# Kernel tuning notes

Hardware: AMD Instinct MI355X
Metric: run time of the kernel (lower is better)

Reference implementation:

```python
import jax, jax.numpy as jnp
import numpy as np

C = 512
NUM_HEADS = 4
GROUPS = 32
EPS = 1e-5


def setup_inputs() -> dict:
    key = jax.random.key(0)
    ks = jax.random.split(key, 7)
    x = jax.random.normal(ks[0], (1, C, 4, 32, 32), dtype=jnp.float32)
    norm_w = jax.random.normal(ks[1], (C,), dtype=jnp.float32) * 0.02 + 1.0
    norm_b = jax.random.normal(ks[2], (C,), dtype=jnp.float32) * 0.02
    # 1x1x1 Conv3d == pointwise linear over channels
    qkv_w = jax.random.normal(ks[3], (3 * C, C), dtype=jnp.float32) * (C ** -0.5)
    qkv_b = jax.random.normal(ks[4], (3 * C,), dtype=jnp.float32) * 0.02
    proj_w = jax.random.normal(ks[5], (C, C), dtype=jnp.float32) * (C ** -0.5)
    proj_b = jax.random.normal(ks[6], (C,), dtype=jnp.float32) * 0.02
    return {"x": x, "norm_w": norm_w, "norm_b": norm_b,
            "qkv_w": qkv_w, "qkv_b": qkv_b,
            "proj_w": proj_w, "proj_b": proj_b}


def reference(x, norm_w, norm_b, qkv_w, qkv_b, proj_w, proj_b):
    B, Cc, T, H, W = x.shape
    N = T * H * W
    nh = NUM_HEADS
    d = Cc // nh
    # GroupNorm(32, C), biased variance, eps=1e-5
    xg = x.reshape(B, GROUPS, Cc // GROUPS, N)
    mu = xg.mean(axis=(2, 3), keepdims=True)
    var = xg.var(axis=(2, 3), keepdims=True)
    h = ((xg - mu) * jax.lax.rsqrt(var + EPS)).reshape(B, Cc, N)
    h = h * norm_w[None, :, None] + norm_b[None, :, None]
    # QKV 1x1 conv as channel matmul: (B, 3C, N)
    qkv = jnp.einsum('oc,bcn->bon', qkv_w, h) + qkv_b[None, :, None]
    qkv = qkv.reshape(B, 3, nh, d, N)
    q, k, v = qkv[:, 0], qkv[:, 1], qkv[:, 2]  # each (B, nh, d, N)
    scale = d ** -0.5
    attn = jax.nn.softmax(jnp.einsum('bhdn,bhdm->bhnm', q, k) * scale, axis=-1)
    out = jnp.einsum('bhnm,bhdm->bhdn', attn, v).reshape(B, Cc, N)
    out = jnp.einsum('oc,bcn->bon', proj_w, out) + proj_b[None, :, None]
    return x + out.reshape(B, Cc, T, H, W)
```

## Files before the change

### kernel.cpp

```cpp
#include <hip/hip_runtime.h>
#include <hip/hip_bf16.h>

#define CDIM 512
#define NTOK 4096
#define NH 4
#define DH 128
#define NGRP 32
#define EPS 1e-5f
#define NSPLIT 4
#define KVBLK 64
#define TPS (NTOK/KVBLK/NSPLIT)

typedef __attribute__((ext_vector_type(8))) short bf16x8;
typedef __attribute__((ext_vector_type(4))) short short4v;
typedef __attribute__((ext_vector_type(4))) float f32x4;
typedef __attribute__((ext_vector_type(16))) float f32x16;
typedef __attribute__((ext_vector_type(2))) unsigned int u32x2;

__device__ inline unsigned short f2bf(float f){
  unsigned int u = __float_as_uint(f);
  u = (u + 0x7fffu + ((u >> 16) & 1u)) >> 16;
  return (unsigned short)u;
}

__device__ inline float bf2f(unsigned short u){
  return __uint_as_float(((unsigned int)u) << 16);
}

__device__ inline f32x4 mfma_bf16(bf16x8 a, bf16x8 b, f32x4 c){
  asm("v_mfma_f32_16x16x32_bf16 %0, %1, %2, %0" : "+v"(c) : "v"(a), "v"(b));
  return c;
}

__device__ inline f32x16 mfma32(bf16x8 a, bf16x8 b, f32x16 c){
  asm("v_mfma_f32_32x32x16_bf16 %0, %1, %2, %0" : "+v"(c) : "v"(a), "v"(b));
  return c;
}

__device__ inline unsigned int cvtpk(float lo, float hi){
  unsigned int r;
  asm("v_cvt_pk_bf16_f32 %0, %1, %2" : "=v"(r) : "v"(lo), "v"(hi));
  return r;
}

#define GLD16(gsrc, ldst) \
  __builtin_amdgcn_global_load_lds((__attribute__((address_space(1))) const void*)(gsrc), \
                                   (__attribute__((address_space(3))) void*)(ldst), 16, 0, 0)

#define KSC (0.088388347648318447f * 1.4426950408889634f)
#define INV_KSC (1.0f / KSC)
#define THR_RAW 60.0f
#define THR_K (THR_RAW * KSC)

__global__ __launch_bounds__(256) void k_convert(const float* __restrict__ qkv_w,
                                                 const float* __restrict__ proj_w,
                                                 unsigned short* __restrict__ qw,
                                                 unsigned short* __restrict__ pw){
  int stride = gridDim.x * blockDim.x;
  int i0 = blockIdx.x * blockDim.x + threadIdx.x;
  for (int i = i0; i < 3*CDIM*CDIM; i += stride) qw[i] = f2bf(qkv_w[i]);
  for (int i = i0; i < CDIM*CDIM; i += stride)   pw[i] = f2bf(proj_w[i]);
}

__global__ __launch_bounds__(256) void k_gnstats(const float* __restrict__ x,
                                                 float* __restrict__ stats){
  const int g = blockIdx.x, t = threadIdx.x;
  const f32x4* p = (const f32x4*)(x + (size_t)g * (16*NTOK));
  float s = 0.f, ss = 0.f;
  for (int i = t; i < 16*NTOK/4; i += 256){
    f32x4 v = p[i];
    s  += v[0]+v[1]+v[2]+v[3];
    ss += v[0]*v[0]+v[1]*v[1]+v[2]*v[2]+v[3]*v[3];
  }
  for (int off = 32; off > 0; off >>= 1){ s += __shfl_down(s, off); ss += __shfl_down(ss, off); }
  __shared__ float rs[4], rss[4];
  if ((t & 63) == 0){ rs[t>>6] = s; rss[t>>6] = ss; }
  __syncthreads();
  if (t == 0){
    float S  = rs[0]+rs[1]+rs[2]+rs[3];
    float SS = rss[0]+rss[1]+rss[2]+rss[3];
    const float inv = 1.f / (float)(16*NTOK);
    float mu  = S * inv;
    float var = SS * inv - mu*mu;
    stats[g]        = mu;
    stats[NGRP + g] = rsqrtf(var + EPS);
  }
}

__global__ __launch_bounds__(256) void k_gnapply(const float* __restrict__ x,
                                                 const float* __restrict__ stats,
                                                 const float* __restrict__ nw,
                                                 const float* __restrict__ nbias,
                                                 unsigned short* __restrict__ h_t){
  __shared__ float tile[64][68];
  const int n0 = blockIdx.x * 64, c0 = blockIdx.y * 64;
  const int t = threadIdx.x;
  {
    const int cl = t >> 2;
    #pragma unroll
    for (int i = 0; i < 4; i++){
      const int f4 = (t & 3) + i*4;
      *(f32x4*)&tile[cl][f4*4] = *(const f32x4*)(x + (size_t)(c0+cl)*NTOK + n0 + f4*4);
    }
  }
  __syncthreads();
  const int nl = t >> 2, cb = (t & 3) * 16;
  unsigned short ov[16] __attribute__((aligned(8)));
  #pragma unroll
  for (int j = 0; j < 16; j++){
    const int c = c0 + cb + j;
    const int grp = c >> 4;
    const float val = (tile[cb+j][nl] - stats[grp]) * stats[NGRP+grp] * nw[c] + nbias[c];
    ov[j] = f2bf(val);
  }
  unsigned short* dst = h_t + (size_t)(n0+nl)*CDIM + c0 + cb;
  #pragma unroll
  for (int j = 0; j < 4; j++) *(short4v*)(dst + j*4) = *(const short4v*)(ov + j*4);
}

template<int MODE>
__global__ __launch_bounds__(256) void k_gemm(const unsigned short* __restrict__ A,
                                              const unsigned short* __restrict__ Bt,
                                              const float* __restrict__ bias,
                                              const float* __restrict__ xres,
                                              unsigned short* __restrict__ q_t,
                                              unsigned short* __restrict__ k_t,
                                              unsigned short* __restrict__ vbuf,
                                              float* __restrict__ out,
                                              int K)
{
  __shared__ unsigned short Asm[128*32];
  __shared__ unsigned short Bsm[128*32];
  const int m0 = blockIdx.y * 128, n0 = blockIdx.x * 128;
  const int t = threadIdx.x;
  const int lane = t & 63, w = t >> 6;
  const int lo = lane & 15, g = lane >> 4;
  const int wr = w >> 1, wc = w & 1;
  f32x4 acc[4][4];
  #pragma unroll
  for (int i=0;i<4;i++)
    #pragma unroll
    for (int j=0;j<4;j++) acc[i][j] = f32x4{0.f,0.f,0.f,0.f};

  const int row = t >> 2, cb8 = (t & 3) * 8;
  for (int k0 = 0; k0 < K; k0 += 32){
    __syncthreads();
    *(bf16x8*)(Asm + row*32 + cb8)      = *(const bf16x8*)(A  + (size_t)(m0+row)*K    + k0 + cb8);
    *(bf16x8*)(Asm + (row+64)*32 + cb8) = *(const bf16x8*)(A  + (size_t)(m0+row+64)*K + k0 + cb8);
    *(bf16x8*)(Bsm + row*32 + cb8)      = *(const bf16x8*)(Bt + (size_t)(n0+row)*K    + k0 + cb8);
    *(bf16x8*)(Bsm + (row+64)*32 + cb8) = *(const bf16x8*)(Bt + (size_t)(n0+row+64)*K + k0 + cb8);
    __syncthreads();
    bf16x8 af[4], bfr[4];
    #pragma unroll
    for (int i=0;i<4;i++) af[i]  = *(const bf16x8*)(Asm + (wr*64 + i*16 + lo)*32 + g*8);
    #pragma unroll
    for (int j=0;j<4;j++) bfr[j] = *(const bf16x8*)(Bsm + (wc*64 + j*16 + lo)*32 + g*8);
    #pragma unroll
    for (int i=0;i<4;i++)
      #pragma unroll
      for (int j=0;j<4;j++)
        acc[i][j] = mfma_bf16(af[i], bfr[j], acc[i][j]);
  }

  if constexpr (MODE == 0){
    const int sQ = m0 >> 9;
    const int hh = (m0 >> 7) & 3;
    #pragma unroll
    for (int i=0;i<4;i++){
      const int ddb = wr*64 + i*16 + g*4;
      const int ob  = m0 + ddb;
      float b[4];
      #pragma unroll
      for (int r=0;r<4;r++) b[r] = bias[ob + r];
      #pragma unroll
      for (int j=0;j<4;j++){
        const int n = n0 + wc*64 + j*16 + lo;
        if (sQ < 2){
          unsigned short pk[4] __attribute__((aligned(8)));
          #pragma unroll
          for (int r=0;r<4;r++) pk[r] = f2bf(acc[i][j][r] + b[r]);
          unsigned short* dst = (sQ == 0 ? q_t : k_t) + ((size_t)hh*NTOK + n)*DH + ddb;
          *(short4v*)dst = *(const short4v*)pk;
        } else {
          #pragma unroll
          for (int r=0;r<4;r++)
            vbuf[((size_t)hh*DH + ddb + r)*NTOK + n] = f2bf(acc[i][j][r] + b[r]);
        }
      }
    }
  } else {
    #pragma unroll
    for (int i=0;i<4;i++){
      const int ob = m0 + wr*64 + i*16 + g*4;
      float b[4];
      #pragma unroll
      for (int r=0;r<4;r++) b[r] = bias[ob + r];
      #pragma unroll
      for (int j=0;j<4;j++){
        const int n = n0 + wc*64 + j*16 + lo;
        #pragma unroll
        for (int r=0;r<4;r++){
          size_t idx = (size_t)(ob + r)*NTOK + n;
          out[idx] = acc[i][j][r] + b[r] + xres[idx];
        }
      }
    }
  }
}

__global__ __launch_bounds__(256, 2) void k_attn(const unsigned short* __restrict__ q_t,
                                                 const unsigned short* __restrict__ k_t,
                                                 const unsigned short* __restrict__ vbuf,
                                                 unsigned short* __restrict__ opart,
                                                 float* __restrict__ mlbuf){
  const int h = blockIdx.y;
  const int qt = blockIdx.x >> 2, split = blockIdx.x & 3;
  const int t = threadIdx.x, w = t >> 6, lane = t & 63;
  const int la = lane & 31, hi = lane >> 5;
  const int s15 = la & 15, s7 = la & 7;
  const int nbq = qt * 128 + w * 32;

  __shared__ __align__(16) unsigned short Ksm[64*128];
  __shared__ __align__(16) unsigned short Vsm[128*64];
  __shared__ __align__(16) unsigned short Pt[4][32][76];

  const unsigned short* kg = k_t  + (size_t)h*NTOK*DH;
  const unsigned short* vg = vbuf + (size_t)h*DH*NTOK;

  auto stage = [&](int mt){
    const unsigned short* kgm = kg + (size_t)mt*KVBLK*DH;
    const unsigned short* vgm = vg + mt*KVBLK;
    #pragma unroll
    for (int rnd = 0; rnd < 4; rnd++){
      const int c = rnd*256 + t;
      const int row = c >> 4, col = c & 15;
      GLD16(kgm + (size_t)row*DH + ((col ^ (row & 15))*8), &Ksm[c*8]);
    }
    #pragma unroll
    for (int rnd = 0; rnd < 4; rnd++){
      const int c = rnd*256 + t;
      const int row = c >> 3, col = c & 7;
      GLD16(vgm + (size_t)row*NTOK + ((col ^ (row & 7))*8), &Vsm[c*8]);
    }
  };

  bf16x8 qa[8];
  {
    const unsigned short* qr = q_t + ((size_t)h*NTOK + nbq + la)*DH + hi*8;
    #pragma unroll
    for (int ks=0;ks<8;ks++) qa[ks] = *(const bf16x8*)(qr + ks*16);
  }

  float mk = -1e30f;
  float lsum = 0.f;
  f32x16 oacc[4];
  #pragma unroll
  for (int dt=0;dt<4;dt++)
    #pragma unroll
    for (int r=0;r<16;r++) oacc[dt][r] = 0.f;

  const int mt0 = split * TPS;
  for (int it = 0; it < TPS; it++){
    __syncthreads();
    stage(mt0 + it);
    __syncthreads();

    const unsigned short* Ks = Ksm;
    const unsigned short* Vs = Vsm;
    unsigned short* Pw = &Pt[w][0][0];

    #pragma unroll
    for (int half = 0; half < 2; half++){
      f32x16 s;
      #pragma unroll
      for (int r=0;r<16;r++) s[r] = 0.f;
      __builtin_amdgcn_s_setprio(1);
      #pragma unroll
      for (int ks=0; ks<8; ks++){
        bf16x8 kf = *(const bf16x8*)(Ks + (half*32 + la)*128 + (((2*ks + hi) ^ s15) * 8));
        s = mfma32(kf, qa[ks], s);
      }
      __builtin_amdgcn_s_setprio(0);
      float hmax = s[0];
      #pragma unroll
      for (int r=1;r<16;r++) hmax = fmaxf(hmax, s[r]);
      hmax = fmaxf(hmax, __shfl_xor(hmax, 32));
      const float hk = hmax * KSC;
      if (!__all(hk <= mk + THR_K)){
        const float mnk = fmaxf(mk, hk);
        const float al  = exp2f(mk - mnk);
        mk = mnk;
        lsum *= al;
        #pragma unroll
        for (int dt=0;dt<4;dt++)
          #pragma unroll
          for (int r=0;r<16;r++) oacc[dt][r] *= al;
      }
      #pragma unroll
      for (int r=0;r<16;r++){
        s[r] = exp2f(fmaf(s[r], KSC, -mk));
        lsum += s[r];
      }
      #pragma unroll
      for (int g2=0; g2<4; g2++){
        u32x2 pk;
        pk[0] = cvtpk(s[4*g2+0], s[4*g2+1]);
        pk[1] = cvtpk(s[4*g2+2], s[4*g2+3]);
        *(u32x2*)(Pw + la*76 + half*32 + 8*g2 + 4*hi) = pk;
      }
      __builtin_amdgcn_wave_barrier();
      __builtin_amdgcn_s_setprio(1);
      #pragma unroll
      for (int kst2=0; kst2<2; kst2++){
        const int kst = half*2 + kst2;
        bf16x8 pb = *(const bf16x8*)(Pw + la*76 + kst*16 + hi*8);
        #pragma unroll
        for (int dt=0; dt<4; dt++){
          bf16x8 vf = *(const bf16x8*)(Vs + (dt*32 + la)*64 + (((2*kst + hi) ^ s7) * 8));
          oacc[dt] = mfma32(vf, pb, oacc[dt]);
        }
      }
      __builtin_amdgcn_s_setprio(0);
    }
  }
  const float lt = lsum + __shfl_xor(lsum, 32);
  const float linv = 1.f / lt;
  unsigned short* Od = opart + ((size_t)(split*NH + h)*NTOK + nbq + la)*DH;
  #pragma unroll
  for (int dt=0;dt<4;dt++)
    #pragma unroll
    for (int g2=0; g2<4; g2++){
      unsigned short pk[4] __attribute__((aligned(8)));
      #pragma unroll
      for (int j=0;j<4;j++) pk[j] = f2bf(oacc[dt][4*g2+j] * linv);
      *(short4v*)(Od + dt*32 + 8*g2 + 4*hi) = *(const short4v*)pk;
    }
  if (hi == 0){
    float* ml = mlbuf + ((size_t)(split*NH + h)*NTOK + nbq)*2;
    ml[la*2]     = mk * INV_KSC;
    ml[la*2 + 1] = lt;
  }
}

__global__ __launch_bounds__(256) void k_merge(const unsigned short* __restrict__ opart,
                                               const float* __restrict__ mlbuf,
                                               unsigned short* __restrict__ ao_t){
  const int h = blockIdx.y;
  const int n = blockIdx.x*2 + (threadIdx.x >> 7);
  const int d = threadIdx.x & 127;
  float ms[NSPLIT], ls[NSPLIT], m = -1e30f;
  #pragma unroll
  for (int s=0;s<NSPLIT;s++){
    const float* ml = mlbuf + ((size_t)(s*NH + h)*NTOK + n)*2;
    ms[s] = ml[0]; ls[s] = ml[1];
    m = fmaxf(m, ms[s]);
  }
  float wsum = 0.f, o = 0.f;
  #pragma unroll
  for (int s=0;s<NSPLIT;s++){
    float wgt = exp2f((ms[s]-m)*KSC) * ls[s];
    wsum += wgt;
    o += wgt * bf2f(opart[((size_t)(s*NH + h)*NTOK + n)*DH + d]);
  }
  ao_t[(size_t)n*CDIM + h*DH + d] = f2bf(o / wsum);
}

extern "C" void kernel_launch(void* const* d_in, const int* in_sizes, int n_in,
                              void* d_out, int out_size, void* d_ws, size_t ws_size,
                              hipStream_t stream){
  const float* x      = (const float*)d_in[0];
  const float* norm_w = (const float*)d_in[1];
  const float* norm_b = (const float*)d_in[2];
  const float* qkv_w  = (const float*)d_in[3];
  const float* qkv_b  = (const float*)d_in[4];
  const float* proj_w = (const float*)d_in[5];
  const float* proj_b = (const float*)d_in[6];
  float* out = (float*)d_out;

  char* ws = (char*)d_ws;
  unsigned short* qw  = (unsigned short*)(ws);
  unsigned short* pw  = (unsigned short*)(ws + 1572864);
  unsigned short* h_t = (unsigned short*)(ws + 2097152);
  unsigned short* q_t = (unsigned short*)(ws + 6291456);
  unsigned short* k_t = (unsigned short*)(ws + 10485760);
  unsigned short* vb  = (unsigned short*)(ws + 14680064);
  unsigned short* ao  = (unsigned short*)(ws + 18874368);
  float* stats        = (float*)(ws + 23068672);
  unsigned short* opart = (unsigned short*)(ws + 23072768);
  float* mlbuf        = (float*)(ws + 39849984);

  hipLaunchKernelGGL(k_convert, dim3(1024), dim3(256), 0, stream, qkv_w, proj_w, qw, pw);
  hipLaunchKernelGGL(k_gnstats, dim3(32), dim3(256), 0, stream, x, stats);
  hipLaunchKernelGGL(k_gnapply, dim3(64, 8), dim3(256), 0, stream, x, stats, norm_w, norm_b, h_t);
  hipLaunchKernelGGL((k_gemm<0>), dim3(32, 12), dim3(256), 0, stream,
                     qw, h_t, qkv_b, (const float*)nullptr,
                     q_t, k_t, vb, (float*)nullptr, 512);
  hipLaunchKernelGGL(k_attn, dim3(32*NSPLIT, NH), dim3(256), 0, stream, q_t, k_t, vb, opart, mlbuf);
  hipLaunchKernelGGL(k_merge, dim3(NTOK/2, NH), dim3(256), 0, stream, opart, mlbuf, ao);
  hipLaunchKernelGGL((k_gemm<1>), dim3(32, 4), dim3(256), 0, stream,
                     pw, ao, proj_b, x,
                     (unsigned short*)nullptr, (unsigned short*)nullptr, (unsigned short*)nullptr, out, 512);
}
```

Baseline: 126.7 us.

## Keep softmax probabilities in registers for PV MFMA and merge prep kernels

The attention kernel no longer writes the probability tile to LDS and reads it back. It rebuilds the bf16 A-operand in registers with cross-half lane shuffles and swaps the MFMA operand order, so the output accumulator is now transposed (query rows across registers). The rescale and final normalisation therefore broadcast per-row factors with shuffles, and the output store becomes scalar 2-byte writes. Separately, the weight-conversion and group-norm stats kernels are merged into one launch to cut launch overhead, with the trade-off of more shuffles and less coalesced stores.

```diff
diff --git a/kernel.cpp b/kernel.cpp
--- a/kernel.cpp
+++ b/kernel.cpp
@@ -15,7 +15,7 @@
 typedef __attribute__((ext_vector_type(4))) short short4v;
 typedef __attribute__((ext_vector_type(4))) float f32x4;
 typedef __attribute__((ext_vector_type(16))) float f32x16;
-typedef __attribute__((ext_vector_type(2))) unsigned int u32x2;
+typedef __attribute__((ext_vector_type(4))) unsigned int u32x4;
 
 __device__ inline unsigned short f2bf(float f){
   unsigned int u = __float_as_uint(f);
@@ -52,38 +52,40 @@
 #define THR_RAW 60.0f
 #define THR_K (THR_RAW * KSC)
 
-__global__ __launch_bounds__(256) void k_convert(const float* __restrict__ qkv_w,
-                                                 const float* __restrict__ proj_w,
-                                                 unsigned short* __restrict__ qw,
-                                                 unsigned short* __restrict__ pw){
-  int stride = gridDim.x * blockDim.x;
-  int i0 = blockIdx.x * blockDim.x + threadIdx.x;
-  for (int i = i0; i < 3*CDIM*CDIM; i += stride) qw[i] = f2bf(qkv_w[i]);
-  for (int i = i0; i < CDIM*CDIM; i += stride)   pw[i] = f2bf(proj_w[i]);
-}
-
-__global__ __launch_bounds__(256) void k_gnstats(const float* __restrict__ x,
-                                                 float* __restrict__ stats){
-  const int g = blockIdx.x, t = threadIdx.x;
-  const f32x4* p = (const f32x4*)(x + (size_t)g * (16*NTOK));
-  float s = 0.f, ss = 0.f;
-  for (int i = t; i < 16*NTOK/4; i += 256){
-    f32x4 v = p[i];
-    s  += v[0]+v[1]+v[2]+v[3];
-    ss += v[0]*v[0]+v[1]*v[1]+v[2]*v[2]+v[3]*v[3];
-  }
-  for (int off = 32; off > 0; off >>= 1){ s += __shfl_down(s, off); ss += __shfl_down(ss, off); }
+__global__ __launch_bounds__(256) void k_prep(const float* __restrict__ qkv_w,
+                                              const float* __restrict__ proj_w,
+                                              unsigned short* __restrict__ qw,
+                                              unsigned short* __restrict__ pw,
+                                              const float* __restrict__ x,
+                                              float* __restrict__ stats){
+  const int t = threadIdx.x;
   __shared__ float rs[4], rss[4];
-  if ((t & 63) == 0){ rs[t>>6] = s; rss[t>>6] = ss; }
-  __syncthreads();
-  if (t == 0){
-    float S  = rs[0]+rs[1]+rs[2]+rs[3];
-    float SS = rss[0]+rss[1]+rss[2]+rss[3];
-    const float inv = 1.f / (float)(16*NTOK);
-    float mu  = S * inv;
-    float var = SS * inv - mu*mu;
-    stats[g]        = mu;
-    stats[NGRP + g] = rsqrtf(var + EPS);
+  if (blockIdx.x < 32){
+    const int g = blockIdx.x;
+    const f32x4* p = (const f32x4*)(x + (size_t)g * (16*NTOK));
+    float s = 0.f, ss = 0.f;
+    for (int i = t; i < 16*NTOK/4; i += 256){
+      f32x4 v = p[i];
+      s  += v[0]+v[1]+v[2]+v[3];
+      ss += v[0]*v[0]+v[1]*v[1]+v[2]*v[2]+v[3]*v[3];
+    }
+    for (int off = 32; off > 0; off >>= 1){ s += __shfl_down(s, off); ss += __shfl_down(ss, off); }
+    if ((t & 63) == 0){ rs[t>>6] = s; rss[t>>6] = ss; }
+    __syncthreads();
+    if (t == 0){
+      float S  = rs[0]+rs[1]+rs[2]+rs[3];
+      float SS = rss[0]+rss[1]+rss[2]+rss[3];
+      const float inv = 1.f / (float)(16*NTOK);
+      float mu  = S * inv;
+      float var = SS * inv - mu*mu;
+      stats[g]        = mu;
+      stats[NGRP + g] = rsqrtf(var + EPS);
+    }
+  } else {
+    const int stride = 1024 * 256;
+    const int i0 = (blockIdx.x - 32) * 256 + t;
+    for (int i = i0; i < 3*CDIM*CDIM; i += stride) qw[i] = f2bf(qkv_w[i]);
+    for (int i = i0; i < CDIM*CDIM; i += stride)   pw[i] = f2bf(proj_w[i]);
   }
 }
 
@@ -222,7 +224,6 @@
 
   __shared__ __align__(16) unsigned short Ksm[64*128];
   __shared__ __align__(16) unsigned short Vsm[128*64];
-  __shared__ __align__(16) unsigned short Pt[4][32][76];
 
   const unsigned short* kg = k_t  + (size_t)h*NTOK*DH;
   const unsigned short* vg = vbuf + (size_t)h*DH*NTOK;
@@ -267,7 +268,6 @@
 
     const unsigned short* Ks = Ksm;
     const unsigned short* Vs = Vsm;
-    unsigned short* Pw = &Pt[w][0][0];
 
     #pragma unroll
     for (int half = 0; half < 2; half++){
@@ -292,49 +292,57 @@
         mk = mnk;
         lsum *= al;
         #pragma unroll
-        for (int dt=0;dt<4;dt++)
+        for (int r=0;r<16;r++){
+          const float a = __shfl(al, (r&3) + 8*(r>>2) + 4*hi);
           #pragma unroll
-          for (int r=0;r<16;r++) oacc[dt][r] *= al;
+          for (int dt=0;dt<4;dt++) oacc[dt][r] *= a;
+        }
       }
       #pragma unroll
       for (int r=0;r<16;r++){
         s[r] = exp2f(fmaf(s[r], KSC, -mk));
         lsum += s[r];
       }
-      #pragma unroll
-      for (int g2=0; g2<4; g2++){
-        u32x2 pk;
-        pk[0] = cvtpk(s[4*g2+0], s[4*g2+1]);
-        pk[1] = cvtpk(s[4*g2+2], s[4*g2+3]);
-        *(u32x2*)(Pw + la*76 + half*32 + 8*g2 + 4*hi) = pk;
-      }
-      __builtin_amdgcn_wave_barrier();
+      bf16x8 paf[2];
+      #pragma unroll
+      for (int b=0;b<2;b++){
+        unsigned int A = cvtpk(s[8*b+0], s[8*b+1]);
+        unsigned int B = cvtpk(s[8*b+2], s[8*b+3]);
+        unsigned int C = cvtpk(s[8*b+4], s[8*b+5]);
+        unsigned int D = cvtpk(s[8*b+6], s[8*b+7]);
+        unsigned int E = hi ? A : C;
+        unsigned int F = hi ? B : D;
+        E = (unsigned int)__shfl_xor((int)E, 32);
+        F = (unsigned int)__shfl_xor((int)F, 32);
+        u32x4 m;
+        m[0] = hi ? E : A;
+        m[1] = hi ? F : B;
+        m[2] = hi ? C : E;
+        m[3] = hi ? D : F;
+        paf[b] = __builtin_bit_cast(bf16x8, m);
+      }
       __builtin_amdgcn_s_setprio(1);
       #pragma unroll
-      for (int kst2=0; kst2<2; kst2++){
-        const int kst = half*2 + kst2;
-        bf16x8 pb = *(const bf16x8*)(Pw + la*76 + kst*16 + hi*8);
-        #pragma unroll
-        for (int dt=0; dt<4; dt++){
-          bf16x8 vf = *(const bf16x8*)(Vs + (dt*32 + la)*64 + (((2*kst + hi) ^ s7) * 8));
-          oacc[dt] = mfma32(vf, pb, oacc[dt]);
-        }
+      for (int dt=0; dt<4; dt++){
+        const int vbase = (dt*32 + la)*64;
+        bf16x8 vf0 = *(const bf16x8*)(Vs + vbase + (((2*(half*2+0) + hi) ^ s7) * 8));
+        bf16x8 vf1 = *(const bf16x8*)(Vs + vbase + (((2*(half*2+1) + hi) ^ s7) * 8));
+        oacc[dt] = mfma32(paf[0], vf0, oacc[dt]);
+        oacc[dt] = mfma32(paf[1], vf1, oacc[dt]);
       }
       __builtin_amdgcn_s_setprio(0);
     }
   }
   const float lt = lsum + __shfl_xor(lsum, 32);
-  const float linv = 1.f / lt;
-  unsigned short* Od = opart + ((size_t)(split*NH + h)*NTOK + nbq + la)*DH;
-  #pragma unroll
-  for (int dt=0;dt<4;dt++)
-    #pragma unroll
-    for (int g2=0; g2<4; g2++){
-      unsigned short pk[4] __attribute__((aligned(8)));
-      #pragma unroll
-      for (int j=0;j<4;j++) pk[j] = f2bf(oacc[dt][4*g2+j] * linv);
-      *(short4v*)(Od + dt*32 + 8*g2 + 4*hi) = *(const short4v*)pk;
-    }
+  unsigned short* Od = opart + ((size_t)(split*NH + h)*NTOK + nbq)*DH;
+  #pragma unroll
+  for (int r=0;r<16;r++){
+    const int q = (r&3) + 8*(r>>2) + 4*hi;
+    const float linv = 1.f / __shfl(lt, q);
+    #pragma unroll
+    for (int dt=0;dt<4;dt++)
+      Od[(size_t)q*DH + dt*32 + la] = f2bf(oacc[dt][r] * linv);
+  }
   if (hi == 0){
     float* ml = mlbuf + ((size_t)(split*NH + h)*NTOK + nbq)*2;
     ml[la*2]     = mk * INV_KSC;
@@ -389,8 +397,7 @@
   unsigned short* opart = (unsigned short*)(ws + 23072768);
   float* mlbuf        = (float*)(ws + 39849984);
 
-  hipLaunchKernelGGL(k_convert, dim3(1024), dim3(256), 0, stream, qkv_w, proj_w, qw, pw);
-  hipLaunchKernelGGL(k_gnstats, dim3(32), dim3(256), 0, stream, x, stats);
+  hipLaunchKernelGGL(k_prep, dim3(1056), dim3(256), 0, stream, qkv_w, proj_w, qw, pw, x, stats);
   hipLaunchKernelGGL(k_gnapply, dim3(64, 8), dim3(256), 0, stream, x, stats, norm_w, norm_b, h_t);
   hipLaunchKernelGGL((k_gemm<0>), dim3(32, 12), dim3(256), 0, stream,
                      qw, h_t, qkv_b, (const float*)nullptr,
```

After: 116.1 us. 8.4% less time.
